# Performance work log

Hardware: AMD Instinct MI355X
Metric: run time of the kernel (lower is better)

Reference implementation:

```python
import jax, jax.numpy as jnp
import numpy as np

NUM_HEADS = 16
HEAD_DIM = 80
DIM = NUM_HEADS * HEAD_DIM
SEQ = 2048
SCALE = HEAD_DIM ** -0.5


def rotate_half(x):
    x1, x2 = jnp.split(x, 2, axis=-1)
    return jnp.concatenate((-x2, x1), axis=-1)


def setup_inputs() -> dict:
    key = jax.random.key(0)
    ks = jax.random.split(key, 8)
    hidden_states = jax.random.normal(ks[0], (SEQ, DIM), dtype=jnp.float32)
    cu_seqlens = jnp.array([0, SEQ], dtype=jnp.int32)  # unused by the math
    # rotary embeddings for head_dim
    inv_freq = 1.0 / (10000.0 ** (jnp.arange(0, HEAD_DIM // 2, dtype=jnp.float32) / (HEAD_DIM // 2)))
    freqs = jnp.outer(jnp.arange(SEQ, dtype=jnp.float32), inv_freq)  # [S, hd/2]
    emb = jnp.concatenate((freqs, freqs), axis=-1)  # [S, hd]
    cos = jnp.cos(emb)
    sin = jnp.sin(emb)
    w_qkv = jax.random.normal(ks[1], (3 * DIM, DIM), dtype=jnp.float32) * (DIM ** -0.5)
    b_qkv = jax.random.normal(ks[2], (3 * DIM,), dtype=jnp.float32) * 0.02
    w_proj = jax.random.normal(ks[3], (DIM, DIM), dtype=jnp.float32) * (DIM ** -0.5)
    b_proj = jax.random.normal(ks[4], (DIM,), dtype=jnp.float32) * 0.02
    return {"hidden_states": hidden_states, "cu_seqlens": cu_seqlens, "cos": cos,
            "sin": sin, "w_qkv": w_qkv, "b_qkv": b_qkv, "w_proj": w_proj, "b_proj": b_proj}


def reference(hidden_states, cu_seqlens, cos, sin, w_qkv, b_qkv, w_proj, b_proj):
    S = hidden_states.shape[0]
    qkv = hidden_states @ w_qkv.T + b_qkv  # [S, 3*D]
    qkv = qkv.reshape(S, 3, NUM_HEADS, HEAD_DIM)
    q, k, v = qkv[:, 0], qkv[:, 1], qkv[:, 2]  # each [S, H, hd]
    c = cos[:, None, :]  # [S, 1, hd]
    s = sin[:, None, :]
    q = q * c + rotate_half(q) * s
    k = k * c + rotate_half(k) * s
    # SDPA, non-causal: [H, S, S]
    scores = jnp.einsum('shd,thd->hst', q, k) * SCALE
    attn = jax.nn.softmax(scores, axis=-1)
    out = jnp.einsum('hst,thd->shd', attn, v).reshape(S, DIM)
    return out @ w_proj.T + b_proj
```

## Files before the change

### kernel.cpp

```cpp
#include <hip/hip_runtime.h>


#define SEQLEN   2048
#define DIMM     1280
#define NHEADS   16
#define HD       80
#define QKV_N    3840
#define NSPLIT   4
#define KVSPAN   (SEQLEN / NSPLIT)
#define QSCALE_LOG2E 0.16130083587064776f

#define KSTRIDE  88
#define VFSTRIDE 24

#define EXP2F(x) __builtin_amdgcn_exp2f(x)

#define GLD16(gptr, lptr)                                                      \
    __builtin_amdgcn_global_load_lds(                                          \
        (const __attribute__((address_space(1))) void*)(gptr),                 \
        (__attribute__((address_space(3))) void*)(lptr), 16, 0, 0)

typedef float f32x4 __attribute__((ext_vector_type(4)));
typedef _Float16 half8 __attribute__((ext_vector_type(8)));
typedef _Float16 half4 __attribute__((ext_vector_type(4)));
typedef _Float16 half2v __attribute__((ext_vector_type(2)));

static __device__ __forceinline__ f32x4 mfma_16x16x32(half8 a, half8 b, f32x4 c) {
    return __builtin_amdgcn_mfma_f32_16x16x32_f16(a, b, c, 0, 0, 0);
}
static __device__ __forceinline__ f32x4 mfma_16x16x16(half4 a, half4 b, f32x4 c) {
    return __builtin_amdgcn_mfma_f32_16x16x16f16(a, b, c, 0, 0, 0);
}
static __device__ __forceinline__ half4 lo4(half8 v) {
    return __builtin_shufflevector(v, v, 0, 1, 2, 3);
}
static __device__ __forceinline__ half4 hi4(half8 v) {
    return __builtin_shufflevector(v, v, 4, 5, 6, 7);
}

__global__ __launch_bounds__(256)
void cast_all(const float* __restrict__ hs, const float* __restrict__ wq,
              const float* __restrict__ wp, _Float16* __restrict__ dhs,
              _Float16* __restrict__ dwq, _Float16* __restrict__ dwp) {
    const int n1 = SEQLEN * DIMM / 4, n2 = QKV_N * DIMM / 4, n3 = DIMM * DIMM / 4;
    int i = blockIdx.x * 256 + threadIdx.x;
    const float4* src; half4* dst; int j;
    if (i < n1)           { src = (const float4*)hs; dst = (half4*)dhs; j = i; }
    else if (i < n1 + n2) { src = (const float4*)wq; dst = (half4*)dwq; j = i - n1; }
    else if (i < n1 + n2 + n3) { src = (const float4*)wp; dst = (half4*)dwp; j = i - n1 - n2; }
    else return;
    const float4 v = src[j];
    half4 h;
    h.x = (_Float16)v.x; h.y = (_Float16)v.y;
    h.z = (_Float16)v.z; h.w = (_Float16)v.w;
    dst[j] = h;
}

template<bool OUT_F16>
__global__ __launch_bounds__(256, 2)
void gemm_bt64(const _Float16* __restrict__ A, const _Float16* __restrict__ B,
               const float* __restrict__ bias, void* __restrict__ Cout,
               int M, int N, int K) {
    __shared__ __align__(16) _Float16 As[2][64 * 32];
    __shared__ __align__(16) _Float16 Bs[2][128 * 32];
    const int tid  = threadIdx.x;
    const int lane = tid & 63;
    const int wave = tid >> 6;
    const int l15  = lane & 15;
    const int quad = lane >> 4;
    const int wm   = wave & 1;
    const int wn   = wave >> 1;
    const long bm = blockIdx.x, bn = blockIdx.y;

    const _Float16* Ag = A + bm * 64 * (long)K;
    const _Float16* Bg = B + bn * 128 * (long)K;

    const int srow = lane >> 2;
    const int scol = (lane & 3) * 8;
    f32x4 acc[2][4] = {};

    for (int k0 = 0; k0 < K; k0 += 64) {
        __syncthreads();
#pragma unroll
        for (int p = 0; p < 2; p++) {
            const int kp = k0 + p * 32;
            const long arow = 16 * wave + srow;
            GLD16(Ag + arow * K + kp + scol, &As[p][512 * wave + lane * 8]);
#pragma unroll
            for (int cc = 0; cc < 2; cc++) {
                const int c = wave + cc * 4;
                const long brow = 16 * c + srow;
                GLD16(Bg + brow * K + kp + scol, &Bs[p][512 * c + lane * 8]);
            }
        }
        __syncthreads();
#pragma unroll
        for (int p = 0; p < 2; p++) {
            half8 af[2], bf[4];
#pragma unroll
            for (int t = 0; t < 2; t++)
                af[t] = *(const half8*)&As[p][(wm * 32 + t * 16 + l15) * 32 + quad * 8];
#pragma unroll
            for (int t = 0; t < 4; t++)
                bf[t] = *(const half8*)&Bs[p][(wn * 64 + t * 16 + l15) * 32 + quad * 8];
#pragma unroll
            for (int mt = 0; mt < 2; mt++)
#pragma unroll
                for (int nt = 0; nt < 4; nt++)
                    acc[mt][nt] = mfma_16x16x32(af[mt], bf[nt], acc[mt][nt]);
        }
    }

    float bv[4];
#pragma unroll
    for (int nt = 0; nt < 4; nt++)
        bv[nt] = bias[bn * 128 + wn * 64 + nt * 16 + l15];

#pragma unroll
    for (int mt = 0; mt < 2; mt++) {
#pragma unroll
        for (int r = 0; r < 4; r++) {
            const long row = bm * 64 + wm * 32 + mt * 16 + quad * 4 + r;
#pragma unroll
            for (int nt = 0; nt < 4; nt++) {
                const long col = bn * 128 + wn * 64 + nt * 16 + l15;
                const float v = acc[mt][nt][r] + bv[nt];
                if (OUT_F16) ((_Float16*)Cout)[row * (long)N + col] = (_Float16)v;
                else         ((float*)Cout)[row * (long)N + col] = v;
            }
        }
    }
}

__global__ __launch_bounds__(256)
void rope_repack_t(const _Float16* __restrict__ qkv,
                   const float* __restrict__ cosb,
                   const float* __restrict__ sinb,
                   _Float16* __restrict__ Qh,
                   _Float16* __restrict__ Kh,
                   _Float16* __restrict__ Vt) {
    const int s0 = blockIdx.x * 64;
    const int h  = blockIdx.y;
    __shared__ __align__(16) _Float16 Ts[64 * 88];
    const int tid = threadIdx.x;

    for (int i = tid; i < 640; i += 256) {
        const int r = i / 10, c = (i - r * 10) * 8;
        *(half8*)&Ts[r * 88 + c] =
            *(const half8*)&qkv[(long)(s0 + r) * QKV_N + 2 * DIMM + h * HD + c];
    }

    for (int i = tid; i < 320; i += 256) {
        const int r = i / 5, d = (i - r * 5) * 8;
        const _Float16* row = qkv + (long)(s0 + r) * QKV_N + h * HD;
        const half8 q0 = *(const half8*)&row[d];
        const half8 q1 = *(const half8*)&row[d + 40];
        const half8 k0 = *(const half8*)&row[DIMM + d];
        const half8 k1 = *(const half8*)&row[DIMM + d + 40];
        const float4 cA = *(const float4*)&cosb[(s0 + r) * HD + d];
        const float4 cB = *(const float4*)&cosb[(s0 + r) * HD + d + 4];
        const float4 sA = *(const float4*)&sinb[(s0 + r) * HD + d];
        const float4 sB = *(const float4*)&sinb[(s0 + r) * HD + d + 4];
        half8 qo0, qo1, ko0, ko1;
#pragma unroll
        for (int j = 0; j < 8; j++) {
            const float cj = (j < 4) ? cA[j] : cB[j - 4];
            const float sj = (j < 4) ? sA[j] : sB[j - 4];
            qo0[j] = (_Float16)(((float)q0[j] * cj - (float)q1[j] * sj) * QSCALE_LOG2E);
            qo1[j] = (_Float16)(((float)q1[j] * cj + (float)q0[j] * sj) * QSCALE_LOG2E);
            ko0[j] = (_Float16)((float)k0[j] * cj - (float)k1[j] * sj);
            ko1[j] = (_Float16)((float)k1[j] * cj + (float)k0[j] * sj);
        }
        const long o = ((long)h * SEQLEN + s0 + r) * HD;
        *(half8*)&Qh[o + d]      = qo0;
        *(half8*)&Qh[o + d + 40] = qo1;
        *(half8*)&Kh[o + d]      = ko0;
        *(half8*)&Kh[o + d + 40] = ko1;
    }
    __syncthreads();
    for (int i = tid; i < 640; i += 256) {
        const int d = i >> 3, sc = (i & 7) * 8;
        half8 v;
#pragma unroll
        for (int j = 0; j < 8; j++) v[j] = Ts[(sc + j) * 88 + d];
        *(half8*)&Vt[((long)h * HD + d) * SEQLEN + s0 + sc] = v;
    }
}

__global__ __launch_bounds__(512, 8)
void attn_kernel(const _Float16* __restrict__ Qh, const _Float16* __restrict__ Kh,
                 const _Float16* __restrict__ Vt,
                 _Float16* __restrict__ Ohat0, _Float16* __restrict__ Ohat1,
                 float* __restrict__ Lpart) {
    const int s0 = blockIdx.x * 128;
    const int h  = blockIdx.y;
    const int z  = blockIdx.z;
    __shared__ __align__(16) _Float16 Ks[64 * KSTRIDE];
    __shared__ __align__(16) _Float16 VF[5 * 64 * VFSTRIDE];

    const int tid  = threadIdx.x;
    const int lane = tid & 63;
    const int wave = tid >> 6;
    const int l15  = lane & 15;
    const int quad = lane >> 4;

    const int zBeg = z * KVSPAN, zEnd = zBeg + KVSPAN;

    const _Float16* Qg = Qh + ((long)h * SEQLEN + s0 + wave * 16 + l15) * HD;
    const half8 qf0 = *(const half8*)&Qg[quad * 8];
    const half8 qf1 = *(const half8*)&Qg[32 + quad * 8];
    const half4 qf2 = *(const half4*)&Qg[64 + quad * 4];

    int offA, lA, offB, lB0, lB1 = 0, offC = 0, lC0 = 0, lC1 = 0;
    {
        const int rA = tid / 10, cA = (tid - rA * 10) * 8;
        offA = rA * HD + cA;
        lA   = rA * KSTRIDE + cA;
        if (tid < 128) {
            const int cB = tid + 512;
            const int rB = cB / 10, ccB = (cB - rB * 10) * 8;
            offB = rB * HD + ccB;
            lB0  = rB * KSTRIDE + ccB;
        } else {
            const int v = tid - 128, d = v >> 3, c8 = (v & 7) * 8;
            offB = d * SEQLEN + c8;
            const int nt = d >> 4, ld = d & 15, ct = c8 >> 4, qb = (c8 & 15) >> 2;
            lB0 = (nt * 64 + qb * 16 + ld) * VFSTRIDE + ct * 4;
            lB1 = (nt * 64 + (qb + 1) * 16 + ld) * VFSTRIDE + ct * 4;
        }
        if (tid < 256) {
            const int v = tid + 384, d = v >> 3, c8 = (v & 7) * 8;
            offC = d * SEQLEN + c8;
            const int nt = d >> 4, ld = d & 15, ct = c8 >> 4, qb = (c8 & 15) >> 2;
            lC0 = (nt * 64 + qb * 16 + ld) * VFSTRIDE + ct * 4;
            lC1 = (nt * 64 + (qb + 1) * 16 + ld) * VFSTRIDE + ct * 4;
        }
    }
    const _Float16* KzBase = Kh + ((long)h * SEQLEN + zBeg) * HD;
    const _Float16* VzBase = Vt + (long)h * HD * SEQLEN + zBeg;

    f32x4 oaccT[5] = {};
    float la0 = 0.f, la1 = 0.f;
    const half2v ones2 = {(_Float16)1.f, (_Float16)1.f};

    for (int t0 = zBeg; t0 < zEnd; t0 += 64) {
        const _Float16* KzT = KzBase + (long)(t0 - zBeg) * HD;
        const _Float16* VzT = VzBase + (t0 - zBeg);
        const half8 a = *(const half8*)(KzT + offA);
        half8 b;
        if (tid < 128) b = *(const half8*)(KzT + offB);
        else           b = *(const half8*)(VzT + offB);
        half8 cv = {};
        if (tid < 256) cv = *(const half8*)(VzT + offC);

        __syncthreads();
        *(half8*)&Ks[lA] = a;
        if (tid < 128) { *(half8*)&Ks[lB0] = b; }
        else {
            *(half4*)&VF[lB0] = lo4(b);
            *(half4*)&VF[lB1] = hi4(b);
        }
        if (tid < 256) {
            *(half4*)&VF[lC0] = lo4(cv);
            *(half4*)&VF[lC1] = hi4(cv);
        }
        __syncthreads();

        f32x4 sa[4] = {};
        __builtin_amdgcn_s_setprio(1);
#pragma unroll
        for (int ct = 0; ct < 4; ct++) {
            const int kb = (ct * 16 + l15) * KSTRIDE;
            const half8 kf0 = *(const half8*)&Ks[kb + quad * 8];
            const half8 kf1 = *(const half8*)&Ks[kb + 32 + quad * 8];
            sa[ct] = mfma_16x16x32(kf0, qf0, sa[ct]);
            sa[ct] = mfma_16x16x32(kf1, qf1, sa[ct]);
            const half4 kf2 = *(const half4*)&Ks[kb + 64 + quad * 4];
            sa[ct] = mfma_16x16x16(kf2, qf2, sa[ct]);
        }
        __builtin_amdgcn_s_setprio(0);

        half4 pb[4];
#pragma unroll
        for (int ct = 0; ct < 4; ct++) {
            const float e0 = EXP2F(sa[ct][0]);
            const float e1 = EXP2F(sa[ct][1]);
            const float e2 = EXP2F(sa[ct][2]);
            const float e3 = EXP2F(sa[ct][3]);
            const half2v p01 = __builtin_bit_cast(half2v, __builtin_amdgcn_cvt_pkrtz(e0, e1));
            const half2v p23 = __builtin_bit_cast(half2v, __builtin_amdgcn_cvt_pkrtz(e2, e3));
            la0 = __builtin_amdgcn_fdot2(p01, ones2, la0, false);
            la1 = __builtin_amdgcn_fdot2(p23, ones2, la1, false);
            pb[ct] = __builtin_shufflevector(p01, p23, 0, 1, 2, 3);
        }

        __builtin_amdgcn_s_setprio(1);
#pragma unroll
        for (int nt = 0; nt < 5; nt++) {
            const half8 va = *(const half8*)&VF[(nt * 64 + lane) * VFSTRIDE];
            const half8 vb = *(const half8*)&VF[(nt * 64 + lane) * VFSTRIDE + 8];
            oaccT[nt] = mfma_16x16x16(lo4(va), pb[0], oaccT[nt]);
            oaccT[nt] = mfma_16x16x16(hi4(va), pb[1], oaccT[nt]);
            oaccT[nt] = mfma_16x16x16(lo4(vb), pb[2], oaccT[nt]);
            oaccT[nt] = mfma_16x16x16(hi4(vb), pb[3], oaccT[nt]);
        }
        __builtin_amdgcn_s_setprio(0);
    }

    float l_acc = la0 + la1;
    l_acc += __shfl_xor(l_acc, 16);
    l_acc += __shfl_xor(l_acc, 32);
    const float inv = 1.0f / l_acc;

    _Float16* Oz = (z < 2) ? Ohat0 : Ohat1;
    const long obase = ((long)(z & 1) * NHEADS + h) * SEQLEN;
    const long lbase = ((long)z * NHEADS + h) * SEQLEN;
    const long row = s0 + wave * 16 + l15;
#pragma unroll
    for (int nt = 0; nt < 5; nt++) {
        half4 o;
#pragma unroll
        for (int r = 0; r < 4; r++) o[r] = (_Float16)(oaccT[nt][r] * inv);
        *(half4*)&Oz[(obase + row) * HD + nt * 16 + quad * 4] = o;
    }
    if (quad == 0)
        Lpart[lbase + row] = l_acc;
}

__global__ __launch_bounds__(256)
void attn_combine(const _Float16* __restrict__ Ohat0,
                  const _Float16* __restrict__ Ohat1,
                  const float* __restrict__ Lp,
                  _Float16* __restrict__ attnb) {
    const int i = blockIdx.x * 256 + threadIdx.x;
    if (i >= SEQLEN * DIMM / 4) return;
    const int flat = i * 4;
    const int s = flat / DIMM;
    const int rem = flat - s * DIMM;
    const int h = rem / HD;
    const int d = rem - h * HD;
    float l[NSPLIT], lsum = 0.f;
#pragma unroll
    for (int zi = 0; zi < NSPLIT; zi++) {
        l[zi] = Lp[((long)zi * NHEADS + h) * SEQLEN + s];
        lsum += l[zi];
    }
    const float invl = 1.0f / lsum;
    float acc[4] = {0.f, 0.f, 0.f, 0.f};
#pragma unroll
    for (int zi = 0; zi < NSPLIT; zi++) {
        const _Float16* Oz = (zi < 2) ? Ohat0 : Ohat1;
        const long obase = ((long)(zi & 1) * NHEADS + h) * SEQLEN;
        const half4 o = *(const half4*)&Oz[(obase + s) * HD + d];
        const float w = l[zi] * invl;
#pragma unroll
        for (int j = 0; j < 4; j++) acc[j] += (float)o[j] * w;
    }
    half4 o;
#pragma unroll
    for (int j = 0; j < 4; j++) o[j] = (_Float16)acc[j];
    *(half4*)&attnb[(long)s * DIMM + rem] = o;
}

extern "C" void kernel_launch(void* const* d_in, const int* in_sizes, int n_in,
                              void* d_out, int out_size, void* d_ws, size_t ws_size,
                              hipStream_t stream) {
    const float* hs     = (const float*)d_in[0];
    const float* cosb   = (const float*)d_in[2];
    const float* sinb   = (const float*)d_in[3];
    const float* w_qkv  = (const float*)d_in[4];
    const float* b_qkv  = (const float*)d_in[5];
    const float* w_proj = (const float*)d_in[6];
    const float* b_proj = (const float*)d_in[7];
    float* out = (float*)d_out;

    _Float16* hsb    = (_Float16*)d_ws;
    _Float16* wqkvb  = hsb    + (long)SEQLEN * DIMM;
    _Float16* wprojb = wqkvb  + (long)QKV_N * DIMM;
    _Float16* qkv    = wprojb + (long)DIMM * DIMM;
    _Float16* Qh     = qkv    + (long)SEQLEN * QKV_N;
    _Float16* Kh     = Qh     + (long)NHEADS * SEQLEN * HD;
    _Float16* Vtb    = Kh     + (long)NHEADS * SEQLEN * HD;
    _Float16* attnb  = Vtb    + (long)NHEADS * HD * SEQLEN;

    _Float16* Ohat0  = (_Float16*)d_ws;
    float*    LpartB = (float*)(Ohat0 + (long)2 * NHEADS * SEQLEN * HD);
    _Float16* Ohat1  = qkv;

    {
        const int ntot = (SEQLEN * DIMM + QKV_N * DIMM + DIMM * DIMM) / 4;
        cast_all<<<(ntot + 255) / 256, 256, 0, stream>>>(
            hs, w_qkv, w_proj, hsb, wqkvb, wprojb);
    }

    gemm_bt64<true><<<dim3(SEQLEN / 64, QKV_N / 128), 256, 0, stream>>>(
        hsb, wqkvb, b_qkv, qkv, SEQLEN, QKV_N, DIMM);

    rope_repack_t<<<dim3(SEQLEN / 64, NHEADS), 256, 0, stream>>>(
        qkv, cosb, sinb, Qh, Kh, Vtb);

    attn_kernel<<<dim3(SEQLEN / 128, NHEADS, NSPLIT), 512, 0, stream>>>(
        Qh, Kh, Vtb, Ohat0, Ohat1, LpartB);

    attn_combine<<<(SEQLEN * DIMM / 4 + 255) / 256, 256, 0, stream>>>(
        Ohat0, Ohat1, LpartB, attnb);

    gemm_bt64<false><<<dim3(SEQLEN / 64, DIMM / 128), 256, 0, stream>>>(
        attnb, wprojb, b_proj, out, SEQLEN, DIMM, DIMM);
}
```

Before: 200.4 us.

## Enlarge QKV GEMM tile and process two query tiles per attention wave

Adds a 128x128-tile GEMM with 512 threads for the QKV projection, so each A and B tile loaded into LDS is reused across more output. The attention kernel now has each wave handle 32 query rows, sharing every LDS K/V fragment across two MFMA chains. This halves K/V staging traffic per query, and the grid is halved to match. In exchange it raises register pressure, lowers occupancy (launch bounds 512,4), and leaves fewer blocks to fill the GPU.

Result: faster. 187.6 us (-6.4%).

```diff
diff --git a/kernel.cpp b/kernel.cpp
--- a/kernel.cpp
+++ b/kernel.cpp
@@ -57,6 +57,77 @@
 }
 
 template<bool OUT_F16>
+__global__ __launch_bounds__(512, 4)
+void gemm_bt128(const _Float16* __restrict__ A, const _Float16* __restrict__ B,
+                const float* __restrict__ bias, void* __restrict__ Cout,
+                int M, int N, int K) {
+    __shared__ __align__(16) _Float16 As[2][128 * 32];
+    __shared__ __align__(16) _Float16 Bs[2][128 * 32];
+    const int tid  = threadIdx.x;
+    const int lane = tid & 63;
+    const int wave = tid >> 6;
+    const int l15  = lane & 15;
+    const int quad = lane >> 4;
+    const int wm   = wave & 3;
+    const int wn   = wave >> 2;
+    const long bm = blockIdx.x, bn = blockIdx.y;
+
+    const _Float16* Ag = A + bm * 128 * (long)K;
+    const _Float16* Bg = B + bn * 128 * (long)K;
+
+    const int srow = lane >> 2;
+    const int scol = (lane & 3) * 8;
+    f32x4 acc[2][4] = {};
+
+    for (int k0 = 0; k0 < K; k0 += 64) {
+        __syncthreads();
+#pragma unroll
+        for (int p = 0; p < 2; p++) {
+            const int kp = k0 + p * 32;
+            const long r = 16 * wave + srow;
+            GLD16(Ag + r * K + kp + scol, &As[p][512 * wave + lane * 8]);
+            GLD16(Bg + r * K + kp + scol, &Bs[p][512 * wave + lane * 8]);
+        }
+        __syncthreads();
+#pragma unroll
+        for (int p = 0; p < 2; p++) {
+            half8 af[2], bf[4];
+#pragma unroll
+            for (int t = 0; t < 2; t++)
+                af[t] = *(const half8*)&As[p][(wm * 32 + t * 16 + l15) * 32 + quad * 8];
+#pragma unroll
+            for (int t = 0; t < 4; t++)
+                bf[t] = *(const half8*)&Bs[p][(wn * 64 + t * 16 + l15) * 32 + quad * 8];
+#pragma unroll
+            for (int mt = 0; mt < 2; mt++)
+#pragma unroll
+                for (int nt = 0; nt < 4; nt++)
+                    acc[mt][nt] = mfma_16x16x32(af[mt], bf[nt], acc[mt][nt]);
+        }
+    }
+
+    float bv[4];
+#pragma unroll
+    for (int nt = 0; nt < 4; nt++)
+        bv[nt] = bias[bn * 128 + wn * 64 + nt * 16 + l15];
+
+#pragma unroll
+    for (int mt = 0; mt < 2; mt++) {
+#pragma unroll
+        for (int r = 0; r < 4; r++) {
+            const long row = bm * 128 + wm * 32 + mt * 16 + quad * 4 + r;
+#pragma unroll
+            for (int nt = 0; nt < 4; nt++) {
+                const long col = bn * 128 + wn * 64 + nt * 16 + l15;
+                const float v = acc[mt][nt][r] + bv[nt];
+                if (OUT_F16) ((_Float16*)Cout)[row * (long)N + col] = (_Float16)v;
+                else         ((float*)Cout)[row * (long)N + col] = v;
+            }
+        }
+    }
+}
+
+template<bool OUT_F16>
 __global__ __launch_bounds__(256, 2)
 void gemm_bt64(const _Float16* __restrict__ A, const _Float16* __restrict__ B,
                const float* __restrict__ bias, void* __restrict__ Cout,
@@ -187,12 +258,12 @@
     }
 }
 
-__global__ __launch_bounds__(512, 8)
+__global__ __launch_bounds__(512, 4)
 void attn_kernel(const _Float16* __restrict__ Qh, const _Float16* __restrict__ Kh,
                  const _Float16* __restrict__ Vt,
                  _Float16* __restrict__ Ohat0, _Float16* __restrict__ Ohat1,
                  float* __restrict__ Lpart) {
-    const int s0 = blockIdx.x * 128;
+    const int s0 = blockIdx.x * 256;
     const int h  = blockIdx.y;
     const int z  = blockIdx.z;
     __shared__ __align__(16) _Float16 Ks[64 * KSTRIDE];
@@ -206,41 +277,45 @@
 
     const int zBeg = z * KVSPAN, zEnd = zBeg + KVSPAN;
 
-    const _Float16* Qg = Qh + ((long)h * SEQLEN + s0 + wave * 16 + l15) * HD;
-    const half8 qf0 = *(const half8*)&Qg[quad * 8];
-    const half8 qf1 = *(const half8*)&Qg[32 + quad * 8];
-    const half4 qf2 = *(const half4*)&Qg[64 + quad * 4];
-
-    int offA, lA, offB, lB0, lB1 = 0, offC = 0, lC0 = 0, lC1 = 0;
+    const _Float16* Qg0 = Qh + ((long)h * SEQLEN + s0 + wave * 32 + l15) * HD;
+    const _Float16* Qg1 = Qg0 + 16 * (long)HD;
+    const half8 qA0 = *(const half8*)&Qg0[quad * 8];
+    const half8 qA1 = *(const half8*)&Qg0[32 + quad * 8];
+    const half4 qA2 = *(const half4*)&Qg0[64 + quad * 4];
+    const half8 qB0 = *(const half8*)&Qg1[quad * 8];
+    const half8 qB1 = *(const half8*)&Qg1[32 + quad * 8];
+    const half4 qB2 = *(const half4*)&Qg1[64 + quad * 4];
+
+    int offA, dsA, offB, dsB0, dsB1 = 0, offC = 0, dsC0 = 0, dsC1 = 0;
     {
         const int rA = tid / 10, cA = (tid - rA * 10) * 8;
         offA = rA * HD + cA;
-        lA   = rA * KSTRIDE + cA;
+        dsA  = rA * KSTRIDE + cA;
         if (tid < 128) {
             const int cB = tid + 512;
             const int rB = cB / 10, ccB = (cB - rB * 10) * 8;
             offB = rB * HD + ccB;
-            lB0  = rB * KSTRIDE + ccB;
+            dsB0 = rB * KSTRIDE + ccB;
         } else {
             const int v = tid - 128, d = v >> 3, c8 = (v & 7) * 8;
             offB = d * SEQLEN + c8;
             const int nt = d >> 4, ld = d & 15, ct = c8 >> 4, qb = (c8 & 15) >> 2;
-            lB0 = (nt * 64 + qb * 16 + ld) * VFSTRIDE + ct * 4;
-            lB1 = (nt * 64 + (qb + 1) * 16 + ld) * VFSTRIDE + ct * 4;
+            dsB0 = (nt * 64 + qb * 16 + ld) * VFSTRIDE + ct * 4;
+            dsB1 = (nt * 64 + (qb + 1) * 16 + ld) * VFSTRIDE + ct * 4;
         }
         if (tid < 256) {
             const int v = tid + 384, d = v >> 3, c8 = (v & 7) * 8;
             offC = d * SEQLEN + c8;
             const int nt = d >> 4, ld = d & 15, ct = c8 >> 4, qb = (c8 & 15) >> 2;
-            lC0 = (nt * 64 + qb * 16 + ld) * VFSTRIDE + ct * 4;
-            lC1 = (nt * 64 + (qb + 1) * 16 + ld) * VFSTRIDE + ct * 4;
+            dsC0 = (nt * 64 + qb * 16 + ld) * VFSTRIDE + ct * 4;
+            dsC1 = (nt * 64 + (qb + 1) * 16 + ld) * VFSTRIDE + ct * 4;
         }
     }
     const _Float16* KzBase = Kh + ((long)h * SEQLEN + zBeg) * HD;
     const _Float16* VzBase = Vt + (long)h * HD * SEQLEN + zBeg;
 
-    f32x4 oaccT[5] = {};
-    float la0 = 0.f, la1 = 0.f;
+    f32x4 oaccA[5] = {}, oaccB[5] = {};
+    float laA0 = 0.f, laA1 = 0.f, laB0 = 0.f, laB1 = 0.f;
     const half2v ones2 = {(_Float16)1.f, (_Float16)1.f};
 
     for (int t0 = zBeg; t0 < zEnd; t0 += 64) {
@@ -254,44 +329,60 @@
         if (tid < 256) cv = *(const half8*)(VzT + offC);
 
         __syncthreads();
-        *(half8*)&Ks[lA] = a;
-        if (tid < 128) { *(half8*)&Ks[lB0] = b; }
+        *(half8*)&Ks[dsA] = a;
+        if (tid < 128) { *(half8*)&Ks[dsB0] = b; }
         else {
-            *(half4*)&VF[lB0] = lo4(b);
-            *(half4*)&VF[lB1] = hi4(b);
+            *(half4*)&VF[dsB0] = lo4(b);
+            *(half4*)&VF[dsB1] = hi4(b);
         }
         if (tid < 256) {
-            *(half4*)&VF[lC0] = lo4(cv);
-            *(half4*)&VF[lC1] = hi4(cv);
+            *(half4*)&VF[dsC0] = lo4(cv);
+            *(half4*)&VF[dsC1] = hi4(cv);
         }
         __syncthreads();
 
-        f32x4 sa[4] = {};
+        f32x4 saA[4] = {}, saB[4] = {};
         __builtin_amdgcn_s_setprio(1);
 #pragma unroll
         for (int ct = 0; ct < 4; ct++) {
             const int kb = (ct * 16 + l15) * KSTRIDE;
             const half8 kf0 = *(const half8*)&Ks[kb + quad * 8];
             const half8 kf1 = *(const half8*)&Ks[kb + 32 + quad * 8];
-            sa[ct] = mfma_16x16x32(kf0, qf0, sa[ct]);
-            sa[ct] = mfma_16x16x32(kf1, qf1, sa[ct]);
             const half4 kf2 = *(const half4*)&Ks[kb + 64 + quad * 4];
-            sa[ct] = mfma_16x16x16(kf2, qf2, sa[ct]);
+            saA[ct] = mfma_16x16x32(kf0, qA0, saA[ct]);
+            saB[ct] = mfma_16x16x32(kf0, qB0, saB[ct]);
+            saA[ct] = mfma_16x16x32(kf1, qA1, saA[ct]);
+            saB[ct] = mfma_16x16x32(kf1, qB1, saB[ct]);
+            saA[ct] = mfma_16x16x16(kf2, qA2, saA[ct]);
+            saB[ct] = mfma_16x16x16(kf2, qB2, saB[ct]);
         }
         __builtin_amdgcn_s_setprio(0);
 
-        half4 pb[4];
+        half4 pbA[4], pbB[4];
 #pragma unroll
         for (int ct = 0; ct < 4; ct++) {
-            const float e0 = EXP2F(sa[ct][0]);
-            const float e1 = EXP2F(sa[ct][1]);
-            const float e2 = EXP2F(sa[ct][2]);
-            const float e3 = EXP2F(sa[ct][3]);
-            const half2v p01 = __builtin_bit_cast(half2v, __builtin_amdgcn_cvt_pkrtz(e0, e1));
-            const half2v p23 = __builtin_bit_cast(half2v, __builtin_amdgcn_cvt_pkrtz(e2, e3));
-            la0 = __builtin_amdgcn_fdot2(p01, ones2, la0, false);
-            la1 = __builtin_amdgcn_fdot2(p23, ones2, la1, false);
-            pb[ct] = __builtin_shufflevector(p01, p23, 0, 1, 2, 3);
+            {
+                const float e0 = EXP2F(saA[ct][0]);
+                const float e1 = EXP2F(saA[ct][1]);
+                const float e2 = EXP2F(saA[ct][2]);
+                const float e3 = EXP2F(saA[ct][3]);
+                const half2v p01 = __builtin_bit_cast(half2v, __builtin_amdgcn_cvt_pkrtz(e0, e1));
+                const half2v p23 = __builtin_bit_cast(half2v, __builtin_amdgcn_cvt_pkrtz(e2, e3));
+                laA0 = __builtin_amdgcn_fdot2(p01, ones2, laA0, false);
+                laA1 = __builtin_amdgcn_fdot2(p23, ones2, laA1, false);
+                pbA[ct] = __builtin_shufflevector(p01, p23, 0, 1, 2, 3);
+            }
+            {
+                const float e0 = EXP2F(saB[ct][0]);
+                const float e1 = EXP2F(saB[ct][1]);
+                const float e2 = EXP2F(saB[ct][2]);
+                const float e3 = EXP2F(saB[ct][3]);
+                const half2v p01 = __builtin_bit_cast(half2v, __builtin_amdgcn_cvt_pkrtz(e0, e1));
+                const half2v p23 = __builtin_bit_cast(half2v, __builtin_amdgcn_cvt_pkrtz(e2, e3));
+                laB0 = __builtin_amdgcn_fdot2(p01, ones2, laB0, false);
+                laB1 = __builtin_amdgcn_fdot2(p23, ones2, laB1, false);
+                pbB[ct] = __builtin_shufflevector(p01, p23, 0, 1, 2, 3);
+            }
         }
 
         __builtin_amdgcn_s_setprio(1);
@@ -299,32 +390,43 @@
         for (int nt = 0; nt < 5; nt++) {
             const half8 va = *(const half8*)&VF[(nt * 64 + lane) * VFSTRIDE];
             const half8 vb = *(const half8*)&VF[(nt * 64 + lane) * VFSTRIDE + 8];
-            oaccT[nt] = mfma_16x16x16(lo4(va), pb[0], oaccT[nt]);
-            oaccT[nt] = mfma_16x16x16(hi4(va), pb[1], oaccT[nt]);
-            oaccT[nt] = mfma_16x16x16(lo4(vb), pb[2], oaccT[nt]);
-            oaccT[nt] = mfma_16x16x16(hi4(vb), pb[3], oaccT[nt]);
+            oaccA[nt] = mfma_16x16x16(lo4(va), pbA[0], oaccA[nt]);
+            oaccB[nt] = mfma_16x16x16(lo4(va), pbB[0], oaccB[nt]);
+            oaccA[nt] = mfma_16x16x16(hi4(va), pbA[1], oaccA[nt]);
+            oaccB[nt] = mfma_16x16x16(hi4(va), pbB[1], oaccB[nt]);
+            oaccA[nt] = mfma_16x16x16(lo4(vb), pbA[2], oaccA[nt]);
+            oaccB[nt] = mfma_16x16x16(lo4(vb), pbB[2], oaccB[nt]);
+            oaccA[nt] = mfma_16x16x16(hi4(vb), pbA[3], oaccA[nt]);
+            oaccB[nt] = mfma_16x16x16(hi4(vb), pbB[3], oaccB[nt]);
         }
         __builtin_amdgcn_s_setprio(0);
     }
 
-    float l_acc = la0 + la1;
-    l_acc += __shfl_xor(l_acc, 16);
-    l_acc += __shfl_xor(l_acc, 32);
-    const float inv = 1.0f / l_acc;
+    float lA = laA0 + laA1, lB = laB0 + laB1;
+    lA += __shfl_xor(lA, 16); lA += __shfl_xor(lA, 32);
+    lB += __shfl_xor(lB, 16); lB += __shfl_xor(lB, 32);
+    const float invA = 1.0f / lA, invB = 1.0f / lB;
 
     _Float16* Oz = (z < 2) ? Ohat0 : Ohat1;
     const long obase = ((long)(z & 1) * NHEADS + h) * SEQLEN;
     const long lbase = ((long)z * NHEADS + h) * SEQLEN;
-    const long row = s0 + wave * 16 + l15;
+    const long rowA = s0 + wave * 32 + l15;
+    const long rowB = rowA + 16;
 #pragma unroll
     for (int nt = 0; nt < 5; nt++) {
-        half4 o;
-#pragma unroll
-        for (int r = 0; r < 4; r++) o[r] = (_Float16)(oaccT[nt][r] * inv);
-        *(half4*)&Oz[(obase + row) * HD + nt * 16 + quad * 4] = o;
-    }
-    if (quad == 0)
-        Lpart[lbase + row] = l_acc;
+        half4 oA, oB;
+#pragma unroll
+        for (int r = 0; r < 4; r++) {
+            oA[r] = (_Float16)(oaccA[nt][r] * invA);
+            oB[r] = (_Float16)(oaccB[nt][r] * invB);
+        }
+        *(half4*)&Oz[(obase + rowA) * HD + nt * 16 + quad * 4] = oA;
+        *(half4*)&Oz[(obase + rowB) * HD + nt * 16 + quad * 4] = oB;
+    }
+    if (quad == 0) {
+        Lpart[lbase + rowA] = lA;
+        Lpart[lbase + rowB] = lB;
+    }
 }
 
 __global__ __launch_bounds__(256)
@@ -393,13 +495,13 @@
             hs, w_qkv, w_proj, hsb, wqkvb, wprojb);
     }
 
-    gemm_bt64<true><<<dim3(SEQLEN / 64, QKV_N / 128), 256, 0, stream>>>(
+    gemm_bt128<true><<<dim3(SEQLEN / 128, QKV_N / 128), 512, 0, stream>>>(
         hsb, wqkvb, b_qkv, qkv, SEQLEN, QKV_N, DIMM);
 
     rope_repack_t<<<dim3(SEQLEN / 64, NHEADS), 256, 0, stream>>>(
         qkv, cosb, sinb, Qh, Kh, Vtb);
 
-    attn_kernel<<<dim3(SEQLEN / 128, NHEADS, NSPLIT), 512, 0, stream>>>(
+    attn_kernel<<<dim3(SEQLEN / 256, NHEADS, NSPLIT), 512, 0, stream>>>(
         Qh, Kh, Vtb, Ohat0, Ohat1, LpartB);
 
     attn_combine<<<(SEQLEN * DIMM / 4 + 255) / 256, 256, 0, stream>>>(
```
